# Kernel optimization log

Measured on AMD Instinct MI355X. Metric: run time of the kernel, lower is better.

The kernel has to match this reference:

```python
import jax, jax.numpy as jnp
import numpy as np

N, E = 50000, 800000
DIN, DH, DOUT, L = 128, 256, 64, 4


def setup_inputs() -> dict:
    key = jax.random.key(0)
    ks = jax.random.split(key, 8)
    x = jax.random.normal(ks[0], (N, DIN), dtype=jnp.float32)
    edge_index = jax.random.randint(ks[1], (2, E), 0, N, dtype=jnp.int64 if jax.config.jax_enable_x64 else jnp.int32)
    W_emb = jax.random.normal(ks[2], (DIN, DH), dtype=jnp.float32) / np.float32(np.sqrt(DIN))
    b_emb = jnp.zeros((DH,), jnp.float32)
    W_conv = jax.random.normal(ks[3], (L, DH, DH), dtype=jnp.float32) / np.float32(np.sqrt(DH))
    b_conv = jnp.zeros((L, DH), jnp.float32)
    W_out = jax.random.normal(ks[4], (DH, DOUT), dtype=jnp.float32) / np.float32(np.sqrt(DH))
    b_out = jnp.zeros((DOUT,), jnp.float32)
    return {"x": x, "edge_index": edge_index, "W_emb": W_emb, "b_emb": b_emb,
            "W_conv": W_conv, "b_conv": b_conv, "W_out": W_out, "b_out": b_out}


def _gcn_layer(h, src, dst, norm, W, b, n):
    # GCNConv: transform, then sym-normalized neighbor aggregation, then bias
    h = h @ W                                  # [N, DH]
    msg = h[src] * norm[:, None]               # [E+N, DH] gather + scale
    return jax.ops.segment_sum(msg, dst, num_segments=n) + b


def reference(x, edge_index, W_emb, b_emb, W_conv, b_conv, W_out, b_out):
    n = x.shape[0]
    loop = jnp.arange(n, dtype=edge_index.dtype)
    src = jnp.concatenate([edge_index[0], loop])   # add self-loops (PyG default)
    dst = jnp.concatenate([edge_index[1], loop])
    deg = jax.ops.segment_sum(jnp.ones_like(src, dtype=x.dtype), dst, num_segments=n)
    dinv = jnp.where(deg > 0, jax.lax.rsqrt(deg), jnp.zeros_like(deg))
    norm = dinv[src] * dinv[dst]                   # per-edge D^-1/2 A D^-1/2 weight
    h = x @ W_emb + b_emb                          # embedding (no activation)
    for i in range(L):                             # small fixed layer count
        h = jnp.tanh(_gcn_layer(h, src, dst, norm, W_conv[i], b_conv[i], n))
    return h @ W_out + b_out
```

## Files before the change

kernel.cpp:

```cpp
#include <hip/hip_runtime.h>
#include <math.h>

#define N_NODES 50000
#define N_EDGES 800000
#define DIN 128
#define DH 256
#define DOUT 64
#define NLAYERS 4

typedef unsigned short u16;
typedef __attribute__((ext_vector_type(8))) _Float16 half8;
typedef __attribute__((ext_vector_type(4))) float f32x4;

__device__ inline u16 f2h(float f) {
  _Float16 h = (_Float16)f;
  return *(u16*)&h;
}
__device__ inline float h2f(u16 u) {
  _Float16 h = *(_Float16*)&u;
  return (float)h;
}


__global__ void k_count(const int* __restrict__ dst, int* __restrict__ cnt, int e) {
  int i = blockIdx.x * blockDim.x + threadIdx.x;
  if (i < e) atomicAdd(&cnt[dst[i]], 1);
}

__global__ void k_scan1(const int* __restrict__ cnt, int* __restrict__ rowptr,
                        int* __restrict__ bsum, float* __restrict__ dinv, int n) {
  __shared__ int sm[256];
  int i = blockIdx.x * 256 + threadIdx.x;
  int v = (i < n) ? cnt[i] : 0;
  if (i < n) dinv[i] = rsqrtf((float)v + 1.0f);
  sm[threadIdx.x] = v;
  __syncthreads();
  for (int off = 1; off < 256; off <<= 1) {
    int t = (threadIdx.x >= off) ? sm[threadIdx.x - off] : 0;
    __syncthreads();
    sm[threadIdx.x] += t;
    __syncthreads();
  }
  if (i < n) rowptr[i + 1] = sm[threadIdx.x];
  if (threadIdx.x == 255) bsum[blockIdx.x] = sm[255];
}

__global__ void k_scan2(int* bsum, int nb) {
  __shared__ int sm[256];
  int v = (threadIdx.x < nb) ? bsum[threadIdx.x] : 0;
  sm[threadIdx.x] = v;
  __syncthreads();
  for (int off = 1; off < 256; off <<= 1) {
    int t = (threadIdx.x >= off) ? sm[threadIdx.x - off] : 0;
    __syncthreads();
    sm[threadIdx.x] += t;
    __syncthreads();
  }
  if (threadIdx.x < nb) bsum[threadIdx.x] = sm[threadIdx.x] - v;
}

__global__ void k_scan3(int* __restrict__ rowptr, const int* __restrict__ bsum,
                        int* __restrict__ cursor, int n) {
  int i = blockIdx.x * 256 + threadIdx.x;
  if (i < n) {
    int v = rowptr[i + 1] + bsum[blockIdx.x];
    rowptr[i + 1] = v;
    if (i + 1 < n) cursor[i + 1] = v;
  }
  if (blockIdx.x == 0 && threadIdx.x == 0) {
    rowptr[0] = 0;
    cursor[0] = 0;
  }
}

__global__ void k_fill(const int* __restrict__ src, const int* __restrict__ dst,
                       const float* __restrict__ dinv,
                       int* __restrict__ cursor, int2* __restrict__ csr, int e) {
  int i = blockIdx.x * blockDim.x + threadIdx.x;
  if (i < e) {
    int d = dst[i], s = src[i];
    int pos = atomicAdd(&cursor[d], 1);
    csr[pos] = make_int2(s, __float_as_int(dinv[s] * dinv[d]));
  }
}

#define X_Q (N_NODES * DIN / 4)
#define W_EMB_SZ (DIN * DH)
#define W_CONV_SZ (DH * DH)
#define W_OUT_SZ (3 * DH * DOUT)
#define W_TOT (W_EMB_SZ + 4 * W_CONV_SZ + W_OUT_SZ)

__global__ void k_convert(const float* __restrict__ x, u16* __restrict__ x_f16,
                          const float* __restrict__ W_emb, const float* __restrict__ W_conv,
                          const float* __restrict__ W_out, u16* __restrict__ Bt_emb,
                          u16* __restrict__ Bt_conv, u16* __restrict__ Bt_out) {
  int i = blockIdx.x * 256 + threadIdx.x;
  if (i < X_Q) {
    float4 v = ((const float4*)x)[i];
    ushort4 o;
    o.x = f2h(v.x); o.y = f2h(v.y); o.z = f2h(v.z); o.w = f2h(v.w);
    ((ushort4*)x_f16)[i] = o;
    return;
  }
  int t = i - X_Q;
  if (t < W_EMB_SZ) {
    int n = t >> 7, k = t & (DIN - 1);
    Bt_emb[t] = f2h(W_emb[k * DH + n]);
  } else if (t < W_EMB_SZ + 4 * W_CONV_SZ) {
    int j = t - W_EMB_SZ;
    int l = j >> 16, jj = j & (W_CONV_SZ - 1);
    int n = jj >> 8, k = jj & (DH - 1);
    Bt_conv[j] = f2h(W_conv[l * W_CONV_SZ + k * DH + n]);
  } else if (t < W_TOT) {
    int j = t - W_EMB_SZ - 4 * W_CONV_SZ;
    int n = j / (3 * DH), kp = j % (3 * DH);
    int k = (kp < DH) ? kp : ((kp < 2 * DH) ? kp - DH : kp - 2 * DH);
    float wv = W_out[k * DOUT + n];
    u16 hiv = f2h(wv);
    u16 v = hiv;
    if (kp >= DH && kp < 2 * DH) v = f2h(wv - h2f(hiv));
    Bt_out[j] = v;
  }
}

template <int NSPLIT, int EPI>
__global__ __launch_bounds__(256) void k_gemm_direct(
    const u16* __restrict__ Ahi, const u16* __restrict__ Alo,
    const u16* __restrict__ Bt, const float* __restrict__ bias,
    float* __restrict__ Cf, u16* __restrict__ Cb, int M, int K, int N) {
  const int lane = threadIdx.x & 63;
  const int w = threadIdx.x >> 6;
  const int q = lane >> 4, r = lane & 15;
  const int ntiles = N >> 6;
  const int mtiles = (M + 63) >> 6;
  int waveId = blockIdx.x * 4 + w;
  if (waveId >= mtiles * ntiles) return;
  int ntile = waveId % ntiles;
  int mtile = waveId / ntiles;
  const int m0 = mtile * 64, n0 = ntile * 64;
  const int Kp = NSPLIT * K;

  int rowA[4];
#pragma unroll
  for (int t = 0; t < 4; t++) {
    int rr = m0 + t * 16 + r;
    rowA[t] = (rr < M) ? rr : (M - 1);
  }

  f32x4 acc[4][4];
#pragma unroll
  for (int t = 0; t < 4; t++)
#pragma unroll
    for (int u = 0; u < 4; u++) acc[t][u] = (f32x4){0.f, 0.f, 0.f, 0.f};

  for (int s = 0; s < NSPLIT; s++) {
    const u16* Aseg = (s == 2) ? Alo : Ahi;
    const u16* Bseg = Bt + s * K;
    for (int kk = 0; kk < K; kk += 32) {
      half8 af[4], bfr[4];
#pragma unroll
      for (int t = 0; t < 4; t++)
        af[t] = *(const half8*)(Aseg + (size_t)rowA[t] * K + kk + q * 8);
#pragma unroll
      for (int u = 0; u < 4; u++)
        bfr[u] = *(const half8*)(Bseg + (size_t)(n0 + u * 16 + r) * Kp + kk + q * 8);
#pragma unroll
      for (int t = 0; t < 4; t++)
#pragma unroll
        for (int u = 0; u < 4; u++)
          acc[t][u] = __builtin_amdgcn_mfma_f32_16x16x32_f16(af[t], bfr[u], acc[t][u], 0, 0, 0);
    }
  }

  float bv[4];
#pragma unroll
  for (int u = 0; u < 4; u++) bv[u] = bias ? bias[n0 + u * 16 + r] : 0.f;

#pragma unroll
  for (int t = 0; t < 4; t++) {
#pragma unroll
    for (int rg = 0; rg < 4; rg++) {
      int row = m0 + t * 16 + q * 4 + rg;
      if (row < M) {
#pragma unroll
        for (int u = 0; u < 4; u++) {
          int col = n0 + u * 16 + r;
          float v = acc[t][u][rg] + bv[u];
          if (EPI == 0)
            Cf[(size_t)row * N + col] = v;
          else
            Cb[(size_t)row * N + col] = f2h(v);
        }
      }
    }
  }
}

__global__ void k_aggregate(const u16* __restrict__ tmph,
                            const int* __restrict__ rowptr, const int2* __restrict__ csr,
                            const float* __restrict__ dinv, const float* __restrict__ bias,
                            u16* __restrict__ hi, u16* __restrict__ lo, int n) {
  int i = (int)((blockIdx.x * (size_t)blockDim.x + threadIdx.x) >> 6);
  int lane = threadIdx.x & 63;
  if (i >= n) return;
  float w0 = dinv[i];
  w0 *= w0;
  const ushort4* T = (const ushort4*)tmph;
  float4 bv = ((const float4*)bias)[lane];
  ushort4 t0 = T[(size_t)i * 64 + lane];
  float ax = bv.x + w0 * h2f(t0.x);
  float ay = bv.y + w0 * h2f(t0.y);
  float az = bv.z + w0 * h2f(t0.z);
  float aw = bv.w + w0 * h2f(t0.w);
  int s = rowptr[i], e = rowptr[i + 1];
  int j = s;
  for (; j + 8 <= e; j += 8) {
    int2 c[8];
    ushort4 v[8];
#pragma unroll
    for (int u = 0; u < 8; u++) c[u] = csr[j + u];
#pragma unroll
    for (int u = 0; u < 8; u++) v[u] = T[(size_t)c[u].x * 64 + lane];
#pragma unroll
    for (int u = 0; u < 8; u++) {
      float f = __int_as_float(c[u].y);
      ax += f * h2f(v[u].x);
      ay += f * h2f(v[u].y);
      az += f * h2f(v[u].z);
      aw += f * h2f(v[u].w);
    }
  }
  for (; j + 4 <= e; j += 4) {
    int2 c[4];
    ushort4 v[4];
#pragma unroll
    for (int u = 0; u < 4; u++) c[u] = csr[j + u];
#pragma unroll
    for (int u = 0; u < 4; u++) v[u] = T[(size_t)c[u].x * 64 + lane];
#pragma unroll
    for (int u = 0; u < 4; u++) {
      float f = __int_as_float(c[u].y);
      ax += f * h2f(v[u].x);
      ay += f * h2f(v[u].y);
      az += f * h2f(v[u].z);
      aw += f * h2f(v[u].w);
    }
  }
  for (; j < e; j++) {
    int2 c = csr[j];
    ushort4 v = T[(size_t)c.x * 64 + lane];
    float f = __int_as_float(c.y);
    ax += f * h2f(v.x);
    ay += f * h2f(v.y);
    az += f * h2f(v.z);
    aw += f * h2f(v.w);
  }
  float ox = tanhf(ax), oy = tanhf(ay), oz = tanhf(az), ow = tanhf(aw);
  size_t base = (size_t)i * DH + lane * 4;
  ushort4 hv;
  hv.x = f2h(ox); hv.y = f2h(oy); hv.z = f2h(oz); hv.w = f2h(ow);
  *(ushort4*)(hi + base) = hv;
  if (lo) {
    ushort4 lv;
    lv.x = f2h(ox - h2f(hv.x));
    lv.y = f2h(oy - h2f(hv.y));
    lv.z = f2h(oz - h2f(hv.z));
    lv.w = f2h(ow - h2f(hv.w));
    *(ushort4*)(lo + base) = lv;
  }
}


extern "C" void kernel_launch(void* const* d_in, const int* in_sizes, int n_in,
                              void* d_out, int out_size, void* d_ws, size_t ws_size,
                              hipStream_t stream) {
  const float* x = (const float*)d_in[0];
  const int* eidx = (const int*)d_in[1];
  const int* esrc = eidx;
  const int* edst = eidx + N_EDGES;
  const float* W_emb = (const float*)d_in[2];
  const float* b_emb = (const float*)d_in[3];
  const float* W_conv = (const float*)d_in[4];
  const float* b_conv = (const float*)d_in[5];
  const float* W_out = (const float*)d_in[6];
  const float* b_out = (const float*)d_in[7];
  float* out = (float*)d_out;

  char* ws = (char*)d_ws;
  size_t off = 0;
  auto alloc = [&](size_t bytes) -> void* {
    void* p = ws + off;
    off += (bytes + 255) & ~(size_t)255;
    return p;
  };
  u16* tmph = (u16*)alloc((size_t)N_NODES * DH * 2);
  u16* h_hi = (u16*)alloc((size_t)N_NODES * DH * 2);
  u16* h_lo = (u16*)alloc((size_t)N_NODES * DH * 2);
  u16* x_f16 = h_lo;
  float* dinv = (float*)alloc((size_t)N_NODES * 4);
  int* cnt = (int*)alloc((size_t)N_NODES * 4);
  int* rowptr = (int*)alloc((size_t)(N_NODES + 1) * 4);
  int* cursor = (int*)alloc((size_t)N_NODES * 4);
  int* bsum = (int*)alloc((size_t)((N_NODES + 255) / 256) * 4);
  int2* csr = (int2*)alloc((size_t)N_EDGES * 8);
  u16* Bt_emb = (u16*)alloc((size_t)W_EMB_SZ * 2);
  u16* Bt_conv = (u16*)alloc((size_t)4 * W_CONV_SZ * 2);
  u16* Bt_out = (u16*)alloc((size_t)W_OUT_SZ * 2);

  int nb = (N_NODES + 255) / 256;
  int eb = (N_EDGES + 255) / 256;

  hipMemsetAsync(cnt, 0, (size_t)N_NODES * 4, stream);
  k_count<<<eb, 256, 0, stream>>>(edst, cnt, N_EDGES);
  k_scan1<<<nb, 256, 0, stream>>>(cnt, rowptr, bsum, dinv, N_NODES);
  k_scan2<<<1, 256, 0, stream>>>(bsum, nb);
  k_scan3<<<nb, 256, 0, stream>>>(rowptr, bsum, cursor, N_NODES);
  k_fill<<<eb, 256, 0, stream>>>(esrc, edst, dinv, cursor, csr, N_EDGES);
  k_convert<<<(X_Q + W_TOT + 255) / 256, 256, 0, stream>>>(x, x_f16, W_emb, W_conv, W_out,
                                                           Bt_emb, Bt_conv, Bt_out);

  int mtiles = (N_NODES + 63) / 64;
  int aggblocks = (N_NODES * 64 + 255) / 256;

  k_gemm_direct<1, 1><<<(mtiles * (DH / 64) + 3) / 4, 256, 0, stream>>>(
      x_f16, nullptr, Bt_emb, b_emb, nullptr, h_hi, N_NODES, DIN, DH);
  for (int l = 0; l < NLAYERS; l++) {
    k_gemm_direct<1, 1><<<(mtiles * (DH / 64) + 3) / 4, 256, 0, stream>>>(
        h_hi, nullptr, Bt_conv + (size_t)l * W_CONV_SZ, nullptr,
        nullptr, tmph, N_NODES, DH, DH);
    k_aggregate<<<aggblocks, 256, 0, stream>>>(tmph, rowptr, csr, dinv,
                                               b_conv + (size_t)l * DH,
                                               h_hi, (l == 3) ? h_lo : nullptr, N_NODES);
  }
  k_gemm_direct<3, 0><<<(mtiles * (DOUT / 64) + 3) / 4, 256, 0, stream>>>(
      h_hi, h_lo, Bt_out, b_out, out, nullptr, N_NODES, DH, DOUT);
}
```

Measured before the change: 612.3 us.

## Stage GEMM tiles in LDS via global_load_lds with 128-row block tiles

Replaces the per-wave direct-from-global MFMA GEMM with a block-tiled GEMM (128 rows by 128 or 64 columns) that stages A and B tiles into shared memory using the global-to-LDS load builtin, so the four waves of a block share each loaded tile. The aim is to cut redundant global and L2 traffic for the dense transforms. The cost is extra barriers per K step, no double buffering, and more LDS use per block. The aggregation kernels, which likely dominate the runtime, are not changed.

```diff
diff --git a/kernel.cpp b/kernel.cpp
--- a/kernel.cpp
+++ b/kernel.cpp
@@ -20,6 +20,11 @@
   _Float16 h = *(_Float16*)&u;
   return (float)h;
 }
+
+#define GLD16(gp, lp)                                                        \
+  __builtin_amdgcn_global_load_lds(                                          \
+      (const __attribute__((address_space(1))) void*)(const void*)(gp),      \
+      (__attribute__((address_space(3))) void*)(void*)(lp), 16, 0, 0)
 
 
 __global__ void k_count(const int* __restrict__ dst, int* __restrict__ cnt, int e) {
@@ -123,69 +128,88 @@
   }
 }
 
-template <int NSPLIT, int EPI>
-__global__ __launch_bounds__(256) void k_gemm_direct(
+template <int BN, int NSPLIT, int EPI>
+__global__ __launch_bounds__(256) void k_gemm_mfma(
     const u16* __restrict__ Ahi, const u16* __restrict__ Alo,
     const u16* __restrict__ Bt, const float* __restrict__ bias,
     float* __restrict__ Cf, u16* __restrict__ Cb, int M, int K, int N) {
-  const int lane = threadIdx.x & 63;
-  const int w = threadIdx.x >> 6;
+  constexpr int BM = 128, BK = 64;
+  constexpr int WN = BN / 2;
+  constexpr int NT = WN / 16;
+  constexpr int BNG = BN / 16;
+  __shared__ u16 As[2 * 8 * 512];
+  __shared__ u16 Bs[2 * BNG * 512];
+  const int tid = threadIdx.x;
+  const int w = tid >> 6, lane = tid & 63;
   const int q = lane >> 4, r = lane & 15;
-  const int ntiles = N >> 6;
-  const int mtiles = (M + 63) >> 6;
-  int waveId = blockIdx.x * 4 + w;
-  if (waveId >= mtiles * ntiles) return;
-  int ntile = waveId % ntiles;
-  int mtile = waveId / ntiles;
-  const int m0 = mtile * 64, n0 = ntile * 64;
+  const int wmg = (w >> 1) * 4;
+  const int wng = (w & 1) * NT;
+  const int m0 = blockIdx.x * BM, n0 = blockIdx.y * BN;
   const int Kp = NSPLIT * K;
-
-  int rowA[4];
+  const int srow = lane & 15;
+  const int sk = (lane >> 4) * 8;
+
+  f32x4 acc[4][NT];
+#pragma unroll
+  for (int t = 0; t < 4; t++)
+#pragma unroll
+    for (int u = 0; u < NT; u++) acc[t][u] = (f32x4){0.f, 0.f, 0.f, 0.f};
+
+  for (int k0 = 0; k0 < Kp; k0 += BK) {
+    const u16* Aptr;
+    int ka;
+    if (NSPLIT == 1) {
+      Aptr = Ahi; ka = k0;
+    } else {
+      Aptr = (k0 < 2 * K) ? Ahi : Alo;
+      ka = (k0 < K) ? k0 : ((k0 < 2 * K) ? (k0 - K) : (k0 - 2 * K));
+    }
+#pragma unroll
+    for (int ii = 0; ii < 4; ii++) {
+      int g = w * 2 + (ii & 1), kb = ii >> 1;
+      int grow = m0 + g * 16 + srow;
+      if (grow > M - 1) grow = M - 1;
+      const u16* gp = Aptr + (size_t)grow * K + ka + kb * 32 + sk;
+      GLD16(gp, &As[(kb * 8 + g) * 512] + (size_t)lane * 8);
+    }
+#pragma unroll
+    for (int ii = 0; ii < BN / 32; ii++) {
+      int g, kb;
+      if (BN == 128) { g = w * 2 + (ii & 1); kb = ii >> 1; }
+      else { g = w; kb = ii; }
+      const u16* gp = Bt + (size_t)(n0 + g * 16 + srow) * Kp + k0 + kb * 32 + sk;
+      GLD16(gp, &Bs[(kb * BNG + g) * 512] + (size_t)lane * 8);
+    }
+    __syncthreads();
+#pragma unroll
+    for (int kb = 0; kb < 2; kb++) {
+      half8 af[4], bfr[NT];
+#pragma unroll
+      for (int t = 0; t < 4; t++)
+        af[t] = *(const half8*)&As[((kb * 8 + wmg + t) * 64 + lane) * 8];
+#pragma unroll
+      for (int u = 0; u < NT; u++)
+        bfr[u] = *(const half8*)&Bs[((kb * BNG + wng + u) * 64 + lane) * 8];
+#pragma unroll
+      for (int t = 0; t < 4; t++)
+#pragma unroll
+        for (int u = 0; u < NT; u++)
+          acc[t][u] = __builtin_amdgcn_mfma_f32_16x16x32_f16(af[t], bfr[u], acc[t][u], 0, 0, 0);
+    }
+    __syncthreads();
+  }
+
 #pragma unroll
   for (int t = 0; t < 4; t++) {
-    int rr = m0 + t * 16 + r;
-    rowA[t] = (rr < M) ? rr : (M - 1);
-  }
-
-  f32x4 acc[4][4];
-#pragma unroll
-  for (int t = 0; t < 4; t++)
-#pragma unroll
-    for (int u = 0; u < 4; u++) acc[t][u] = (f32x4){0.f, 0.f, 0.f, 0.f};
-
-  for (int s = 0; s < NSPLIT; s++) {
-    const u16* Aseg = (s == 2) ? Alo : Ahi;
-    const u16* Bseg = Bt + s * K;
-    for (int kk = 0; kk < K; kk += 32) {
-      half8 af[4], bfr[4];
-#pragma unroll
-      for (int t = 0; t < 4; t++)
-        af[t] = *(const half8*)(Aseg + (size_t)rowA[t] * K + kk + q * 8);
-#pragma unroll
-      for (int u = 0; u < 4; u++)
-        bfr[u] = *(const half8*)(Bseg + (size_t)(n0 + u * 16 + r) * Kp + kk + q * 8);
-#pragma unroll
-      for (int t = 0; t < 4; t++)
-#pragma unroll
-        for (int u = 0; u < 4; u++)
-          acc[t][u] = __builtin_amdgcn_mfma_f32_16x16x32_f16(af[t], bfr[u], acc[t][u], 0, 0, 0);
-    }
-  }
-
-  float bv[4];
-#pragma unroll
-  for (int u = 0; u < 4; u++) bv[u] = bias ? bias[n0 + u * 16 + r] : 0.f;
-
-#pragma unroll
-  for (int t = 0; t < 4; t++) {
 #pragma unroll
     for (int rg = 0; rg < 4; rg++) {
-      int row = m0 + t * 16 + q * 4 + rg;
+      int row = m0 + (w >> 1) * 64 + t * 16 + q * 4 + rg;
       if (row < M) {
 #pragma unroll
-        for (int u = 0; u < 4; u++) {
-          int col = n0 + u * 16 + r;
-          float v = acc[t][u][rg] + bv[u];
+        for (int u = 0; u < NT; u++) {
+          int col = n0 + (w & 1) * WN + u * 16 + r;
+          float v = acc[t][u][rg];
+          if (bias) v += bias[col];
           if (EPI == 0)
             Cf[(size_t)row * N + col] = v;
           else
@@ -319,19 +343,26 @@
   k_convert<<<(X_Q + W_TOT + 255) / 256, 256, 0, stream>>>(x, x_f16, W_emb, W_conv, W_out,
                                                            Bt_emb, Bt_conv, Bt_out);
 
-  int mtiles = (N_NODES + 63) / 64;
+  int mblocks = (N_NODES + 127) / 128;
   int aggblocks = (N_NODES * 64 + 255) / 256;
 
-  k_gemm_direct<1, 1><<<(mtiles * (DH / 64) + 3) / 4, 256, 0, stream>>>(
-      x_f16, nullptr, Bt_emb, b_emb, nullptr, h_hi, N_NODES, DIN, DH);
+  {
+    dim3 g(mblocks, DH / 128);
+    k_gemm_mfma<128, 1, 1><<<g, 256, 0, stream>>>(x_f16, nullptr, Bt_emb, b_emb,
+                                                  nullptr, h_hi, N_NODES, DIN, DH);
+  }
   for (int l = 0; l < NLAYERS; l++) {
-    k_gemm_direct<1, 1><<<(mtiles * (DH / 64) + 3) / 4, 256, 0, stream>>>(
-        h_hi, nullptr, Bt_conv + (size_t)l * W_CONV_SZ, nullptr,
-        nullptr, tmph, N_NODES, DH, DH);
+    dim3 g(mblocks, DH / 128);
+    k_gemm_mfma<128, 1, 1><<<g, 256, 0, stream>>>(h_hi, nullptr,
+                                                  Bt_conv + (size_t)l * W_CONV_SZ, nullptr,
+                                                  nullptr, tmph, N_NODES, DH, DH);
     k_aggregate<<<aggblocks, 256, 0, stream>>>(tmph, rowptr, csr, dinv,
                                                b_conv + (size_t)l * DH,
                                                h_hi, (l == 3) ? h_lo : nullptr, N_NODES);
   }
-  k_gemm_direct<3, 0><<<(mtiles * (DOUT / 64) + 3) / 4, 256, 0, stream>>>(
-      h_hi, h_lo, Bt_out, b_out, out, nullptr, N_NODES, DH, DOUT);
-}
+  {
+    dim3 g(mblocks, 1);
+    k_gemm_mfma<64, 3, 0><<<g, 256, 0, stream>>>(h_hi, h_lo, Bt_out, b_out,
+                                                 out, nullptr, N_NODES, DH, DOUT);
+  }
+}
```

Measured after the change: 566.7 us. 7.5% less time.
